# Kernel tuning notes

Hardware: AMD Instinct MI355X
Metric: run time of the kernel (lower is better)

## Reference

```python
import jax, jax.numpy as jnp
import numpy as np

N = 100000          # num nodes
E = 1600000         # num edges
EMB = 192           # embedding_dimension (divisible by 3)
THIRD = EMB // 3    # 64
NUM_REL = 2
SLOPE = 0.01        # LeakyReLU default negative slope


def leaky_relu(x):
    return jnp.where(x >= 0, x, SLOPE * x)


def setup_inputs() -> dict:
    key = jax.random.key(0)
    ks = jax.random.split(key, 20)
    s = 0.02
    inp = {
        "des": jax.random.normal(ks[0], (N, 768), jnp.float32),
        "tweet": jax.random.normal(ks[1], (N, 768), jnp.float32),
        "num_prop": jax.random.normal(ks[2], (N, 4), jnp.float32),
        "cat_prop": jax.random.normal(ks[3], (N, 3), jnp.float32),
        "edge_index": jax.random.randint(ks[4], (2, E), 0, N, jnp.int64).astype(jnp.int32),
        "edge_type": jax.random.randint(ks[5], (E,), 0, NUM_REL, jnp.int32),
        # params
        "W_des": s * jax.random.normal(ks[6], (768, THIRD), jnp.float32),
        "b_des": jnp.zeros((THIRD,), jnp.float32),
        "W_num": s * jax.random.normal(ks[7], (4, THIRD), jnp.float32),
        "b_num": jnp.zeros((THIRD,), jnp.float32),
        "W_cat": s * jax.random.normal(ks[8], (3, THIRD), jnp.float32),
        "b_cat": jnp.zeros((THIRD,), jnp.float32),
        "W_in": s * jax.random.normal(ks[9], (EMB, EMB), jnp.float32),
        "b_in": jnp.zeros((EMB,), jnp.float32),
        "W_root": s * jax.random.normal(ks[10], (EMB, EMB), jnp.float32),
        "W_rel": s * jax.random.normal(ks[11], (NUM_REL, EMB, EMB), jnp.float32),
        "b_rgcn": jnp.zeros((EMB,), jnp.float32),
        "W_o1": s * jax.random.normal(ks[12], (EMB, EMB), jnp.float32),
        "b_o1": jnp.zeros((EMB,), jnp.float32),
        "W_o2": s * jax.random.normal(ks[13], (EMB, 2), jnp.float32),
        "b_o2": jnp.zeros((2,), jnp.float32),
    }
    return inp


def rgcn_conv(x, edge_index, edge_type, W_root, W_rel, b_rgcn):
    # PyG RGCNConv (default): out = x @ W_root + b + sum_r mean_{edges r -> i}(x[src] @ W_r)
    # mean of (x_j @ W_r) == (mean of x_j) @ W_r, so aggregate first (cheaper).
    src, dst = edge_index[0], edge_index[1]
    h = x[src]  # [E, EMB] gather
    out = x @ W_root + b_rgcn
    for r in range(NUM_REL):
        m = (edge_type == r).astype(x.dtype)  # [E]
        s = jax.ops.segment_sum(h * m[:, None], dst, num_segments=N)  # [N, EMB]
        cnt = jax.ops.segment_sum(m, dst, num_segments=N)             # [N]
        agg = s / jnp.maximum(cnt, 1.0)[:, None]
        out = out + agg @ W_rel[r]
    return out


def reference(des, tweet, num_prop, cat_prop, edge_index, edge_type,
              W_des, b_des, W_num, b_num, W_cat, b_cat, W_in, b_in,
              W_root, W_rel, b_rgcn, W_o1, b_o1, W_o2, b_o2):
    d = leaky_relu(des @ W_des + b_des)
    n = leaky_relu(num_prop @ W_num + b_num)
    c = leaky_relu(cat_prop @ W_cat + b_cat)
    x = jnp.concatenate((d, n, c), axis=1)          # [N, EMB]
    x = leaky_relu(x @ W_in + b_in)
    x = rgcn_conv(x, edge_index, edge_type, W_root, W_rel, b_rgcn)
    # dropout in eval mode = identity
    x = rgcn_conv(x, edge_index, edge_type, W_root, W_rel, b_rgcn)
    x = leaky_relu(x @ W_o1 + b_o1)
    x = x @ W_o2 + b_o2                              # [N, 2]
    return x
```

## Files before the change

### kernel.cpp

```cpp
#include <hip/hip_runtime.h>

typedef _Float16 f16;
typedef _Float16 f16x4 __attribute__((ext_vector_type(4)));
typedef _Float16 f16x8 __attribute__((ext_vector_type(8)));
typedef float f32x4 __attribute__((ext_vector_type(4)));

#define LRELU(v) ((v) >= 0.f ? (v) : 0.01f * (v))

__device__ __forceinline__ int swz(int a) { return a ^ (((a >> 7) & 7) << 4); }

#define BCAP 64

__global__ __launch_bounds__(256) void setup_kernel(
    const float* __restrict__ num_prop, const float* __restrict__ cat_prop,
    const float* __restrict__ W_num, const float* __restrict__ b_num,
    const float* __restrict__ W_cat, const float* __restrict__ b_cat,
    const float* __restrict__ W_des, const float* __restrict__ W_in,
    const float* __restrict__ W_root, const float* __restrict__ W_rel,
    const float* __restrict__ W_o1,
    f16* __restrict__ x0, int* __restrict__ cursor,
    f16* __restrict__ WtDes, f16* __restrict__ WtIn, f16* __restrict__ WtR,
    f16* __restrict__ WtO1,
    int N, int nbf, int nbz)
{
  int b = blockIdx.x;
  int tid = threadIdx.x;
  if (b < nbf) {
    int w = (b * 256 + tid) >> 6;
    int lane = tid & 63;
    if (w < N) {
      const float* npr = num_prop + (size_t)w * 4;
      const float* cpr = cat_prop + (size_t)w * 3;
      float vn = b_num[lane];
#pragma unroll
      for (int k = 0; k < 4; k++) vn += npr[k] * W_num[k * 64 + lane];
      float vc = b_cat[lane];
#pragma unroll
      for (int k = 0; k < 3; k++) vc += cpr[k] * W_cat[k * 64 + lane];
      vn = LRELU(vn);
      vc = LRELU(vc);
      x0[(size_t)w * 192 + 64 + lane] = (f16)vn;
      x0[(size_t)w * 192 + 128 + lane] = (f16)vc;
    }
    return;
  }
  b -= nbf;
  if (b < nbz) {
    int i = b * 256 + tid;
    if (i < N) cursor[i] = 0;
    return;
  }
  b -= nbz;
  if (b < 192) {
    int idx = b * 256 + tid;
    if (idx < 64 * 768) { int n = idx / 768, k = idx % 768; WtDes[idx] = (f16)W_des[k * 64 + n]; }
    return;
  }
  b -= 192;
  if (b < 144) {
    int idx = b * 256 + tid;
    if (idx < 192 * 192) { int n = idx / 192, k = idx % 192; WtIn[idx] = (f16)W_in[k * 192 + n]; }
    return;
  }
  b -= 144;
  if (b < 432) {
    int idx = b * 256 + tid;
    if (idx < 192 * 576) {
      int n = idx / 576, k = idx % 576;
      int seg = k / 192, kk = k % 192;
      float v = (seg == 0) ? W_root[kk * 192 + n] : W_rel[(seg - 1) * 192 * 192 + kk * 192 + n];
      WtR[idx] = (f16)v;
    }
    return;
  }
  b -= 432;
  {
    int idx = b * 256 + tid;
    if (idx < 192 * 192) { int n = idx / 192, k = idx % 192; WtO1[idx] = (f16)W_o1[k * 192 + n]; }
  }
}

__global__ __launch_bounds__(256) void count_fill(
    const int* __restrict__ ei, const int* __restrict__ et,
    int* __restrict__ cursor, int* __restrict__ bucket, int E)
{
  int e = blockIdx.x * 256 + threadIdx.x;
  if (e >= E) return;
  int src = ei[e];
  int dst = ei[E + e];
  int r = et[e];
  int pos = atomicAdd(&cursor[dst], 1);
  if (pos < BCAP) bucket[(size_t)dst * BCAP + pos] = src | (r << 31);
}

__global__ __launch_bounds__(256) void gemm_des_kernel(
    const float* __restrict__ A, const f16* __restrict__ Bt,
    const float* __restrict__ bias, f16* __restrict__ C, int M)
{
  __shared__ f16 lA[128 * 64];
  __shared__ f16 lB[64 * 64];
  const int tid = threadIdx.x, lane = tid & 63, wid = tid >> 6;
  const int wm = wid >> 1, wn = wid & 1;
  const int m0 = blockIdx.x * 128;
  f32x4 acc[4][2] = {};
  const int arow = tid >> 1, ahalf = tid & 1;
  int agr = m0 + arow;
  if (agr >= M) agr = M - 1;
  const float* asrc = A + (size_t)agr * 768 + ahalf * 32;
  for (int k0 = 0; k0 < 768; k0 += 64) {
    {
      const float4* s4 = reinterpret_cast<const float4*>(asrc + k0);
#pragma unroll
      for (int i = 0; i < 4; i++) {
        float4 u = s4[2 * i], w = s4[2 * i + 1];
        f16x8 h;
        h[0] = (f16)u.x; h[1] = (f16)u.y; h[2] = (f16)u.z; h[3] = (f16)u.w;
        h[4] = (f16)w.x; h[5] = (f16)w.y; h[6] = (f16)w.z; h[7] = (f16)w.w;
        int boff = arow * 128 + ahalf * 64 + i * 16;
        *reinterpret_cast<f16x8*>((char*)lA + swz(boff)) = h;
      }
    }
    {
#pragma unroll
      for (int i = 0; i < 2; i++) {
        int c = tid + i * 256;
        int n = c >> 3, k8 = c & 7;
        f16x8 h = *reinterpret_cast<const f16x8*>(Bt + (size_t)n * 768 + k0 + k8 * 8);
        *reinterpret_cast<f16x8*>((char*)lB + swz(n * 128 + k8 * 16)) = h;
      }
    }
    __syncthreads();
#pragma unroll
    for (int ks = 0; ks < 2; ks++) {
      f16x8 af[4], bf[2];
#pragma unroll
      for (int fm = 0; fm < 4; fm++) {
        int row = wm * 64 + fm * 16 + (lane & 15);
        af[fm] = *reinterpret_cast<const f16x8*>((const char*)lA + swz(row * 128 + ks * 64 + (lane >> 4) * 16));
      }
#pragma unroll
      for (int fn = 0; fn < 2; fn++) {
        int nn = wn * 32 + fn * 16 + (lane & 15);
        bf[fn] = *reinterpret_cast<const f16x8*>((const char*)lB + swz(nn * 128 + ks * 64 + (lane >> 4) * 16));
      }
#pragma unroll
      for (int fm = 0; fm < 4; fm++)
#pragma unroll
        for (int fn = 0; fn < 2; fn++)
          acc[fm][fn] = __builtin_amdgcn_mfma_f32_16x16x32_f16(af[fm], bf[fn], acc[fm][fn], 0, 0, 0);
    }
    __syncthreads();
  }
#pragma unroll
  for (int fm = 0; fm < 4; fm++) {
#pragma unroll
    for (int fn = 0; fn < 2; fn++) {
      int gc = wn * 32 + fn * 16 + (lane & 15);
      float b = bias[gc];
#pragma unroll
      for (int r = 0; r < 4; r++) {
        int gr = m0 + wm * 64 + fm * 16 + (lane >> 4) * 4 + r;
        if (gr < M) {
          float v = acc[fm][fn][r] + b;
          C[(size_t)gr * 192 + gc] = (f16)LRELU(v);
        }
      }
    }
  }
}

template <int NSEG, bool RELU, bool OUT2>
__global__ __launch_bounds__(512) void gemm_x_kernel(
    const f16* __restrict__ A0, const f16* __restrict__ A1, const f16* __restrict__ A2,
    const f16* __restrict__ Bt, const float* __restrict__ bias,
    f16* __restrict__ C, int M,
    const float* __restrict__ W_o2, const float* __restrict__ b_o2,
    float* __restrict__ out)
{
  __shared__ f16 lA[128 * 64];
  __shared__ f16 lB[192 * 64];
  const int tid = threadIdx.x, lane = tid & 63, wid = tid >> 6;
  const int wm = wid >> 2, wn = wid & 3;
  const int m0 = blockIdx.x * 128;
  const int Ktot = NSEG * 192;
  f32x4 acc[4][3] = {};
  const f16* segs[3] = {A0, A1, A2};
  const int arow = tid >> 2, aq = tid & 3;
  int agr = m0 + arow;
  if (agr >= M) agr = M - 1;
  int seg = 0, kin = 0;
  for (int it = 0; it < NSEG * 3; it++) {
    {
      const f16x8* s8 = reinterpret_cast<const f16x8*>(segs[seg] + (size_t)agr * 192 + kin + aq * 16);
      f16x8 h0 = s8[0], h1 = s8[1];
      int b0 = arow * 128 + aq * 32;
      *reinterpret_cast<f16x8*>((char*)lA + swz(b0)) = h0;
      *reinterpret_cast<f16x8*>((char*)lA + swz(b0 + 16)) = h1;
    }
    {
      int kb = it * 64;
#pragma unroll
      for (int i = 0; i < 3; i++) {
        int c = tid + i * 512;
        int n = c >> 3, k8 = c & 7;
        f16x8 h = *reinterpret_cast<const f16x8*>(Bt + (size_t)n * Ktot + kb + k8 * 8);
        *reinterpret_cast<f16x8*>((char*)lB + swz(n * 128 + k8 * 16)) = h;
      }
    }
    __syncthreads();
#pragma unroll
    for (int ks = 0; ks < 2; ks++) {
      f16x8 af[4], bf[3];
#pragma unroll
      for (int fm = 0; fm < 4; fm++) {
        int row = wm * 64 + fm * 16 + (lane & 15);
        af[fm] = *reinterpret_cast<const f16x8*>((const char*)lA + swz(row * 128 + ks * 64 + (lane >> 4) * 16));
      }
#pragma unroll
      for (int fn = 0; fn < 3; fn++) {
        int nn = wn * 48 + fn * 16 + (lane & 15);
        bf[fn] = *reinterpret_cast<const f16x8*>((const char*)lB + swz(nn * 128 + ks * 64 + (lane >> 4) * 16));
      }
#pragma unroll
      for (int fm = 0; fm < 4; fm++)
#pragma unroll
        for (int fn = 0; fn < 3; fn++)
          acc[fm][fn] = __builtin_amdgcn_mfma_f32_16x16x32_f16(af[fm], bf[fn], acc[fm][fn], 0, 0, 0);
    }
    __syncthreads();
    kin += 64;
    if (kin == 192) { kin = 0; if (seg < NSEG - 1) seg++; }
  }
  if (OUT2) {
    __shared__ float red[128][2];
    for (int i = tid; i < 256; i += 512) ((float*)red)[i] = 0.f;
    __syncthreads();
    float bb[3], w2v[3][2];
#pragma unroll
    for (int fn = 0; fn < 3; fn++) {
      int gc = wn * 48 + fn * 16 + (lane & 15);
      bb[fn] = bias[gc];
      w2v[fn][0] = W_o2[gc * 2 + 0];
      w2v[fn][1] = W_o2[gc * 2 + 1];
    }
#pragma unroll
    for (int fm = 0; fm < 4; fm++) {
#pragma unroll
      for (int r = 0; r < 4; r++) {
        float p0 = 0.f, p1 = 0.f;
#pragma unroll
        for (int fn = 0; fn < 3; fn++) {
          float v = acc[fm][fn][r] + bb[fn];
          v = LRELU(v);
          p0 += v * w2v[fn][0];
          p1 += v * w2v[fn][1];
        }
#pragma unroll
        for (int m = 1; m < 16; m <<= 1) { p0 += __shfl_xor(p0, m); p1 += __shfl_xor(p1, m); }
        if ((lane & 15) == 0) {
          int lr = wm * 64 + fm * 16 + (lane >> 4) * 4 + r;
          atomicAdd(&red[lr][0], p0);
          atomicAdd(&red[lr][1], p1);
        }
      }
    }
    __syncthreads();
    if (tid < 256) {
      int gr = m0 + (tid >> 1);
      if (gr < M) out[(size_t)gr * 2 + (tid & 1)] = red[tid >> 1][tid & 1] + b_o2[tid & 1];
    }
  } else {
#pragma unroll
    for (int fm = 0; fm < 4; fm++) {
#pragma unroll
      for (int fn = 0; fn < 3; fn++) {
        int gc = wn * 48 + fn * 16 + (lane & 15);
        float b = bias[gc];
#pragma unroll
        for (int r = 0; r < 4; r++) {
          int gr = m0 + wm * 64 + fm * 16 + (lane >> 4) * 4 + r;
          if (gr < M) {
            float v = acc[fm][fn][r] + b;
            if (RELU) v = LRELU(v);
            C[(size_t)gr * 192 + gc] = (f16)v;
          }
        }
      }
    }
  }
}

__global__ __launch_bounds__(256) void agg_kernel(
    const f16* __restrict__ x, const int* __restrict__ bucket,
    const int* __restrict__ cursor,
    f16* __restrict__ agg0, f16* __restrict__ agg1, int N)
{
  int w = (blockIdx.x << 2) + (threadIdx.x >> 6);
  if (w >= N) return;
  const int lane = threadIdx.x & 63;
  const int g = lane >> 4, sub = lane & 15;
  int deg = cursor[w];
  if (deg > BCAP) deg = BCAP;
  const int4* bk4 = reinterpret_cast<const int4*>(bucket + (size_t)w * BCAP);
  float a0[12] = {}, a1[12] = {};
  float c1 = 0.f;
  int nj = (deg + 15) >> 4;
  for (int j = 0; j < nj; ++j) {
    int4 ee = bk4[j * 4 + g];
#pragma unroll
    for (int i = 0; i < 4; ++i) {
      int idx = j * 16 + g * 4 + i;
      if (idx < deg) {
        int e = (i == 0) ? ee.x : (i == 1) ? ee.y : (i == 2) ? ee.z : ee.w;
        int src = e & 0x7fffffff;
        const f16* rowp = x + (size_t)src * 192 + sub * 4;
        f16x4 v0 = *reinterpret_cast<const f16x4*>(rowp);
        f16x4 v1 = *reinterpret_cast<const f16x4*>(rowp + 64);
        f16x4 v2 = *reinterpret_cast<const f16x4*>(rowp + 128);
        float f[12];
#pragma unroll
        for (int c = 0; c < 4; ++c) {
          f[c] = (float)v0[c]; f[4 + c] = (float)v1[c]; f[8 + c] = (float)v2[c];
        }
        if (e < 0) {
          c1 += 1.f;
#pragma unroll
          for (int c = 0; c < 12; ++c) a1[c] += f[c];
        } else {
#pragma unroll
          for (int c = 0; c < 12; ++c) a0[c] += f[c];
        }
      }
    }
  }
#pragma unroll
  for (int c = 0; c < 12; ++c) {
    a0[c] += __shfl_xor(a0[c], 16); a0[c] += __shfl_xor(a0[c], 32);
    a1[c] += __shfl_xor(a1[c], 16); a1[c] += __shfl_xor(a1[c], 32);
  }
  c1 += __shfl_xor(c1, 16); c1 += __shfl_xor(c1, 32);
  float c0 = (float)deg - c1;
  float i0 = 1.f / fmaxf(c0, 1.f);
  float i1 = 1.f / fmaxf(c1, 1.f);
  if (g == 0) {
    f16x4 o0[3], o1[3];
#pragma unroll
    for (int c = 0; c < 12; ++c) {
      o0[c >> 2][c & 3] = (f16)(a0[c] * i0);
      o1[c >> 2][c & 3] = (f16)(a1[c] * i1);
    }
#pragma unroll
    for (int c = 0; c < 3; ++c) {
      *reinterpret_cast<f16x4*>(agg0 + (size_t)w * 192 + c * 64 + sub * 4) = o0[c];
      *reinterpret_cast<f16x4*>(agg1 + (size_t)w * 192 + c * 64 + sub * 4) = o1[c];
    }
  }
}

extern "C" void kernel_launch(void* const* d_in, const int* in_sizes, int n_in,
                              void* d_out, int out_size, void* d_ws, size_t ws_size,
                              hipStream_t stream)
{
  const float* des      = (const float*)d_in[0];
  const float* num_prop = (const float*)d_in[2];
  const float* cat_prop = (const float*)d_in[3];
  const int* edge_index = (const int*)d_in[4];
  const int* edge_type  = (const int*)d_in[5];
  const float* W_des = (const float*)d_in[6];
  const float* b_des = (const float*)d_in[7];
  const float* W_num = (const float*)d_in[8];
  const float* b_num = (const float*)d_in[9];
  const float* W_cat = (const float*)d_in[10];
  const float* b_cat = (const float*)d_in[11];
  const float* W_in  = (const float*)d_in[12];
  const float* b_in  = (const float*)d_in[13];
  const float* W_root= (const float*)d_in[14];
  const float* W_rel = (const float*)d_in[15];
  const float* b_rgcn= (const float*)d_in[16];
  const float* W_o1  = (const float*)d_in[17];
  const float* b_o1  = (const float*)d_in[18];
  const float* W_o2  = (const float*)d_in[19];
  const float* b_o2  = (const float*)d_in[20];
  float* out = (float*)d_out;

  const int N = in_sizes[2] / 4;
  const int E = in_sizes[5];
  (void)n_in; (void)out_size; (void)ws_size;

  char* base = (char*)d_ws;
  size_t off = 0;
  auto take = [&](size_t bytes) -> void* {
    void* p = base + off;
    off += (bytes + 255) & ~(size_t)255;
    return p;
  };
  f16* xA     = (f16*)take((size_t)N * 192 * 2);
  f16* xB     = (f16*)take((size_t)N * 192 * 2);
  f16* agg0   = (f16*)take((size_t)N * 192 * 2);
  f16* agg1   = (f16*)take((size_t)N * 192 * 2);
  int* bucket = (int*)take((size_t)N * BCAP * 4);
  int* cursor = (int*)take((size_t)N * 4);
  f16* WtDes  = (f16*)take(64 * 768 * 2);
  f16* WtIn   = (f16*)take(192 * 192 * 2);
  f16* WtR    = (f16*)take(192 * 576 * 2);
  f16* WtO1   = (f16*)take(192 * 192 * 2);

  const int nbf = (N + 3) / 4;
  const int nbz = (N + 255) / 256;
  const int nsetup = nbf + nbz + 192 + 144 + 432 + 144;
  setup_kernel<<<nsetup, 256, 0, stream>>>(
      num_prop, cat_prop, W_num, b_num, W_cat, b_cat,
      W_des, W_in, W_root, W_rel, W_o1,
      xA, cursor, WtDes, WtIn, WtR, WtO1, N, nbf, nbz);
  count_fill<<<(E + 255) / 256, 256, 0, stream>>>(edge_index, edge_type, cursor, bucket, E);
  gemm_des_kernel<<<(N + 127) / 128, 256, 0, stream>>>(des, WtDes, b_des, xA, N);
  gemm_x_kernel<1, true, false><<<(N + 127) / 128, 512, 0, stream>>>(
      xA, xA, xA, WtIn, b_in, xB, N, nullptr, nullptr, nullptr);
  agg_kernel<<<(N + 3) / 4, 256, 0, stream>>>(xB, bucket, cursor, agg0, agg1, N);
  gemm_x_kernel<3, false, false><<<(N + 127) / 128, 512, 0, stream>>>(
      xB, agg0, agg1, WtR, b_rgcn, xA, N, nullptr, nullptr, nullptr);
  agg_kernel<<<(N + 3) / 4, 256, 0, stream>>>(xA, bucket, cursor, agg0, agg1, N);
  gemm_x_kernel<3, false, false><<<(N + 127) / 128, 512, 0, stream>>>(
      xA, agg0, agg1, WtR, b_rgcn, xB, N, nullptr, nullptr, nullptr);
  gemm_x_kernel<1, false, true><<<(N + 127) / 128, 512, 0, stream>>>(
      xB, xB, xB, WtO1, b_o1, nullptr, N, W_o2, b_o2, out);
}
```

Measured before the change: 557.9 us.

## Fuse RGCN neighbor aggregation into the root/relation GEMM via shared memory

Replaces the separate aggregation kernel and the 3-segment GEMM with one kernel per RGCN layer. Each block first does the root GEMM, then gathers neighbor means one 64-column slice at a time into shared memory and runs the matching relation-weight MFMA steps. The weight layout is permuted to interleave the two relations per slice. This removes the agg0/agg1 round-trip through global memory, but it runs the gather with 8 waves per 128-row tile and stalls on syncthreads, which may lower latency hiding and occupancy for the irregular gathers.

Measured after the change: 1.499 ms. 2.69x slower.

```diff
diff --git a/kernel.cpp b/kernel.cpp
--- a/kernel.cpp
+++ b/kernel.cpp
@@ -67,8 +67,16 @@
     int idx = b * 256 + tid;
     if (idx < 192 * 576) {
       int n = idx / 576, k = idx % 576;
-      int seg = k / 192, kk = k % 192;
-      float v = (seg == 0) ? W_root[kk * 192 + n] : W_rel[(seg - 1) * 192 * 192 + kk * 192 + n];
+      float v;
+      if (k < 192) {
+        v = W_root[k * 192 + n];
+      } else {
+        int q = k - 192;
+        int p = q >> 7, r = q & 127;
+        int rel = (r >= 64) ? 1 : 0;
+        int kk = p * 64 + (r & 63);
+        v = W_rel[rel * 192 * 192 + kk * 192 + n];
+      }
       WtR[idx] = (f16)v;
     }
     return;
@@ -275,7 +283,7 @@
 #pragma unroll
       for (int fn = 0; fn < 3; fn++) {
         int gc = wn * 48 + fn * 16 + (lane & 15);
-        float b = bias[gc];
+        float b = bias[fn * 0 + gc];
 #pragma unroll
         for (int r = 0; r < 4; r++) {
           int gr = m0 + wm * 64 + fm * 16 + (lane >> 4) * 4 + r;
@@ -290,69 +298,142 @@
   }
 }
 
-__global__ __launch_bounds__(256) void agg_kernel(
-    const f16* __restrict__ x, const int* __restrict__ bucket,
-    const int* __restrict__ cursor,
-    f16* __restrict__ agg0, f16* __restrict__ agg1, int N)
+__global__ __launch_bounds__(512) void rgcn_fused_kernel(
+    const f16* __restrict__ X, const int* __restrict__ bucket,
+    const int* __restrict__ cursor, const f16* __restrict__ Bt,
+    const float* __restrict__ bias, f16* __restrict__ C, int M)
 {
-  int w = (blockIdx.x << 2) + (threadIdx.x >> 6);
-  if (w >= N) return;
-  const int lane = threadIdx.x & 63;
+  __shared__ char smem[32768 + 24576];
+  f16* lA = (f16*)smem;
+  f16* lB = (f16*)(smem + 32768);
+  const int tid = threadIdx.x, lane = tid & 63, wid = tid >> 6;
+  const int wm = wid >> 2, wn = wid & 3;
+  const int m0 = blockIdx.x * 128;
+  f32x4 acc[4][3] = {};
+  const int arow = tid >> 2, aq = tid & 3;
+  int agr = m0 + arow;
+  if (agr >= M) agr = M - 1;
   const int g = lane >> 4, sub = lane & 15;
-  int deg = cursor[w];
-  if (deg > BCAP) deg = BCAP;
-  const int4* bk4 = reinterpret_cast<const int4*>(bucket + (size_t)w * BCAP);
-  float a0[12] = {}, a1[12] = {};
-  float c1 = 0.f;
-  int nj = (deg + 15) >> 4;
-  for (int j = 0; j < nj; ++j) {
-    int4 ee = bk4[j * 4 + g];
-#pragma unroll
-    for (int i = 0; i < 4; ++i) {
-      int idx = j * 16 + g * 4 + i;
-      if (idx < deg) {
-        int e = (i == 0) ? ee.x : (i == 1) ? ee.y : (i == 2) ? ee.z : ee.w;
-        int src = e & 0x7fffffff;
-        const f16* rowp = x + (size_t)src * 192 + sub * 4;
-        f16x4 v0 = *reinterpret_cast<const f16x4*>(rowp);
-        f16x4 v1 = *reinterpret_cast<const f16x4*>(rowp + 64);
-        f16x4 v2 = *reinterpret_cast<const f16x4*>(rowp + 128);
-        float f[12];
+
+  auto stage_lB = [&](int it) {
+#pragma unroll
+    for (int i = 0; i < 3; i++) {
+      int c = tid + i * 512;
+      int n = c >> 3, k8 = c & 7;
+      f16x8 h = *reinterpret_cast<const f16x8*>(Bt + (size_t)n * 576 + it * 64 + k8 * 8);
+      *reinterpret_cast<f16x8*>((char*)lB + swz(n * 128 + k8 * 16)) = h;
+    }
+  };
+  auto mfma_step = [&](const char* abase) {
+#pragma unroll
+    for (int ks = 0; ks < 2; ks++) {
+      f16x8 af[4], bf[3];
+#pragma unroll
+      for (int fm = 0; fm < 4; fm++) {
+        int row = wm * 64 + fm * 16 + (lane & 15);
+        af[fm] = *reinterpret_cast<const f16x8*>(abase + swz(row * 128 + ks * 64 + (lane >> 4) * 16));
+      }
+#pragma unroll
+      for (int fn = 0; fn < 3; fn++) {
+        int nn = wn * 48 + fn * 16 + (lane & 15);
+        bf[fn] = *reinterpret_cast<const f16x8*>((const char*)lB + swz(nn * 128 + ks * 64 + (lane >> 4) * 16));
+      }
+#pragma unroll
+      for (int fm = 0; fm < 4; fm++)
+#pragma unroll
+        for (int fn = 0; fn < 3; fn++)
+          acc[fm][fn] = __builtin_amdgcn_mfma_f32_16x16x32_f16(af[fm], bf[fn], acc[fm][fn], 0, 0, 0);
+    }
+  };
+
+  for (int it = 0; it < 3; ++it) {
+    {
+      const f16x8* s8 = reinterpret_cast<const f16x8*>(X + (size_t)agr * 192 + it * 64 + aq * 16);
+      f16x8 h0 = s8[0], h1 = s8[1];
+      int b0 = arow * 128 + aq * 32;
+      *reinterpret_cast<f16x8*>((char*)lA + swz(b0)) = h0;
+      *reinterpret_cast<f16x8*>((char*)lA + swz(b0 + 16)) = h1;
+    }
+    stage_lB(it);
+    __syncthreads();
+    mfma_step((const char*)lA);
+    __syncthreads();
+  }
+
+  for (int p = 0; p < 3; ++p) {
+    for (int pass = 0; pass < 16; ++pass) {
+      int dl = (pass << 3) + wid;
+      int d = m0 + dl;
+      int deg = 0;
+      if (d < M) { deg = cursor[d]; if (deg > BCAP) deg = BCAP; }
+      const int4* bk4 = reinterpret_cast<const int4*>(bucket + (size_t)d * BCAP);
+      float a0[4] = {}, a1[4] = {};
+      float c1f = 0.f;
+      int nj = (deg + 15) >> 4;
+      for (int j = 0; j < nj; ++j) {
+        int4 ee = bk4[j * 4 + g];
+#pragma unroll
+        for (int i = 0; i < 4; ++i) {
+          int idx = j * 16 + g * 4 + i;
+          if (idx < deg) {
+            int e = (i == 0) ? ee.x : (i == 1) ? ee.y : (i == 2) ? ee.z : ee.w;
+            int src = e & 0x7fffffff;
+            f16x4 v = *reinterpret_cast<const f16x4*>(X + (size_t)src * 192 + p * 64 + sub * 4);
+            if (e < 0) {
+              c1f += 1.f;
+#pragma unroll
+              for (int c = 0; c < 4; ++c) a1[c] += (float)v[c];
+            } else {
+#pragma unroll
+              for (int c = 0; c < 4; ++c) a0[c] += (float)v[c];
+            }
+          }
+        }
+      }
+#pragma unroll
+      for (int c = 0; c < 4; ++c) {
+        a0[c] += __shfl_xor(a0[c], 16); a0[c] += __shfl_xor(a0[c], 32);
+        a1[c] += __shfl_xor(a1[c], 16); a1[c] += __shfl_xor(a1[c], 32);
+      }
+      c1f += __shfl_xor(c1f, 16); c1f += __shfl_xor(c1f, 32);
+      if (g == 0) {
+        float c0f = (float)deg - c1f;
+        float i0 = 1.f / fmaxf(c0f, 1.f);
+        float i1 = 1.f / fmaxf(c1f, 1.f);
+        f16x4 o0, o1;
 #pragma unroll
         for (int c = 0; c < 4; ++c) {
-          f[c] = (float)v0[c]; f[4 + c] = (float)v1[c]; f[8 + c] = (float)v2[c];
-        }
-        if (e < 0) {
-          c1 += 1.f;
-#pragma unroll
-          for (int c = 0; c < 12; ++c) a1[c] += f[c];
-        } else {
-#pragma unroll
-          for (int c = 0; c < 12; ++c) a0[c] += f[c];
-        }
-      }
-    }
-  }
-#pragma unroll
-  for (int c = 0; c < 12; ++c) {
-    a0[c] += __shfl_xor(a0[c], 16); a0[c] += __shfl_xor(a0[c], 32);
-    a1[c] += __shfl_xor(a1[c], 16); a1[c] += __shfl_xor(a1[c], 32);
-  }
-  c1 += __shfl_xor(c1, 16); c1 += __shfl_xor(c1, 32);
-  float c0 = (float)deg - c1;
-  float i0 = 1.f / fmaxf(c0, 1.f);
-  float i1 = 1.f / fmaxf(c1, 1.f);
-  if (g == 0) {
-    f16x4 o0[3], o1[3];
-#pragma unroll
-    for (int c = 0; c < 12; ++c) {
-      o0[c >> 2][c & 3] = (f16)(a0[c] * i0);
-      o1[c >> 2][c & 3] = (f16)(a1[c] * i1);
-    }
-#pragma unroll
-    for (int c = 0; c < 3; ++c) {
-      *reinterpret_cast<f16x4*>(agg0 + (size_t)w * 192 + c * 64 + sub * 4) = o0[c];
-      *reinterpret_cast<f16x4*>(agg1 + (size_t)w * 192 + c * 64 + sub * 4) = o1[c];
+          o0[c] = (f16)(a0[c] * i0);
+          o1[c] = (f16)(a1[c] * i1);
+        }
+        int boff = dl * 128 + sub * 8;
+        *reinterpret_cast<f16x4*>((char*)lA + swz(boff)) = o0;
+        *reinterpret_cast<f16x4*>((char*)lA + 16384 + swz(boff)) = o1;
+      }
+    }
+#pragma unroll
+    for (int s = 0; s < 2; ++s) {
+      stage_lB(3 + p * 2 + s);
+      __syncthreads();
+      mfma_step((const char*)lA + s * 16384);
+      __syncthreads();
+    }
+  }
+
+#pragma unroll
+  for (int fm = 0; fm < 4; fm++) {
+#pragma unroll
+    for (int fn = 0; fn < 3; fn++) {
+      int gc = wn * 48 + fn * 16 + (lane & 15);
+      float b = bias[gc];
+#pragma unroll
+      for (int r = 0; r < 4; r++) {
+        int gr = m0 + wm * 64 + fm * 16 + (lane >> 4) * 4 + r;
+        if (gr < M) {
+          float v = acc[fm][fn][r] + b;
+          C[(size_t)gr * 192 + gc] = (f16)v;
+        }
+      }
     }
   }
 }
@@ -396,8 +477,6 @@
   };
   f16* xA     = (f16*)take((size_t)N * 192 * 2);
   f16* xB     = (f16*)take((size_t)N * 192 * 2);
-  f16* agg0   = (f16*)take((size_t)N * 192 * 2);
-  f16* agg1   = (f16*)take((size_t)N * 192 * 2);
   int* bucket = (int*)take((size_t)N * BCAP * 4);
   int* cursor = (int*)take((size_t)N * 4);
   f16* WtDes  = (f16*)take(64 * 768 * 2);
@@ -416,12 +495,10 @@
   gemm_des_kernel<<<(N + 127) / 128, 256, 0, stream>>>(des, WtDes, b_des, xA, N);
   gemm_x_kernel<1, true, false><<<(N + 127) / 128, 512, 0, stream>>>(
       xA, xA, xA, WtIn, b_in, xB, N, nullptr, nullptr, nullptr);
-  agg_kernel<<<(N + 3) / 4, 256, 0, stream>>>(xB, bucket, cursor, agg0, agg1, N);
-  gemm_x_kernel<3, false, false><<<(N + 127) / 128, 512, 0, stream>>>(
-      xB, agg0, agg1, WtR, b_rgcn, xA, N, nullptr, nullptr, nullptr);
-  agg_kernel<<<(N + 3) / 4, 256, 0, stream>>>(xA, bucket, cursor, agg0, agg1, N);
-  gemm_x_kernel<3, false, false><<<(N + 127) / 128, 512, 0, stream>>>(
-      xA, agg0, agg1, WtR, b_rgcn, xB, N, nullptr, nullptr, nullptr);
+  rgcn_fused_kernel<<<(N + 127) / 128, 512, 0, stream>>>(
+      xB, bucket, cursor, WtR, b_rgcn, xA, N);
+  rgcn_fused_kernel<<<(N + 127) / 128, 512, 0, stream>>>(
+      xA, bucket, cursor, WtR, b_rgcn, xB, N);
   gemm_x_kernel<1, false, true><<<(N + 127) / 128, 512, 0, stream>>>(
       xB, xB, xB, WtO1, b_o1, nullptr, N, W_o2, b_o2, out);
 }
```

## Fuse edge bucketing into des GEMM launch and accumulate aggregation in fp16

Applied to the files above, without the earlier changes.

The edge count/fill pass and the des projection GEMM are merged into one launch, with trailing blocks doing the atomic bucket fill. This lets the atomic-heavy scatter overlap with the bandwidth-heavy GEMM and removes one launch. The aggregation kernel now accumulates neighbor rows in packed fp16 vectors instead of converting to fp32, which cuts conversion and ALU work and register use. In exchange, sums over up to 64 neighbors are less precise, and the fused kernel carries GEMM shared-memory allocation on the fill blocks, which can lower their occupancy.

Result: faster. 487.8 us (-12.6%).

```diff
diff --git a/kernel.cpp b/kernel.cpp
--- a/kernel.cpp
+++ b/kernel.cpp
@@ -8,6 +8,14 @@
 #define LRELU(v) ((v) >= 0.f ? (v) : 0.01f * (v))
 
 __device__ __forceinline__ int swz(int a) { return a ^ (((a >> 7) & 7) << 4); }
+
+__device__ __forceinline__ f16x4 shflx4(f16x4 v, int m) {
+  union { f16x4 h; int i[2]; } u;
+  u.h = v;
+  u.i[0] = __shfl_xor(u.i[0], m);
+  u.i[1] = __shfl_xor(u.i[1], m);
+  return u.h;
+}
 
 #define BCAP 64
 
@@ -80,25 +88,25 @@
   }
 }
 
-__global__ __launch_bounds__(256) void count_fill(
+__global__ __launch_bounds__(256) void cfdes_kernel(
+    const float* __restrict__ A, const f16* __restrict__ Bt,
+    const float* __restrict__ bias, f16* __restrict__ C, int M,
     const int* __restrict__ ei, const int* __restrict__ et,
-    int* __restrict__ cursor, int* __restrict__ bucket, int E)
-{
-  int e = blockIdx.x * 256 + threadIdx.x;
-  if (e >= E) return;
-  int src = ei[e];
-  int dst = ei[E + e];
-  int r = et[e];
-  int pos = atomicAdd(&cursor[dst], 1);
-  if (pos < BCAP) bucket[(size_t)dst * BCAP + pos] = src | (r << 31);
-}
-
-__global__ __launch_bounds__(256) void gemm_des_kernel(
-    const float* __restrict__ A, const f16* __restrict__ Bt,
-    const float* __restrict__ bias, f16* __restrict__ C, int M)
+    int* __restrict__ cursor, int* __restrict__ bucket, int E, int nbDES)
 {
   __shared__ f16 lA[128 * 64];
   __shared__ f16 lB[64 * 64];
+  if ((int)blockIdx.x >= nbDES) {
+    int e = ((int)blockIdx.x - nbDES) * 256 + threadIdx.x;
+    if (e < E) {
+      int src = ei[e];
+      int dst = ei[E + e];
+      int r = et[e];
+      int pos = atomicAdd(&cursor[dst], 1);
+      if (pos < BCAP) bucket[(size_t)dst * BCAP + pos] = src | (r << 31);
+    }
+    return;
+  }
   const int tid = threadIdx.x, lane = tid & 63, wid = tid >> 6;
   const int wm = wid >> 1, wn = wid & 1;
   const int m0 = blockIdx.x * 128;
@@ -302,8 +310,8 @@
   int deg = cursor[w];
   if (deg > BCAP) deg = BCAP;
   const int4* bk4 = reinterpret_cast<const int4*>(bucket + (size_t)w * BCAP);
-  float a0[12] = {}, a1[12] = {};
-  float c1 = 0.f;
+  f16x4 a0[3] = {}, a1[3] = {};
+  float c1f = 0.f;
   int nj = (deg + 15) >> 4;
   for (int j = 0; j < nj; ++j) {
     int4 ee = bk4[j * 4 + g];
@@ -317,42 +325,35 @@
         f16x4 v0 = *reinterpret_cast<const f16x4*>(rowp);
         f16x4 v1 = *reinterpret_cast<const f16x4*>(rowp + 64);
         f16x4 v2 = *reinterpret_cast<const f16x4*>(rowp + 128);
-        float f[12];
-#pragma unroll
-        for (int c = 0; c < 4; ++c) {
-          f[c] = (float)v0[c]; f[4 + c] = (float)v1[c]; f[8 + c] = (float)v2[c];
+        if (e < 0) {
+          c1f += 1.f;
+          a1[0] += v0; a1[1] += v1; a1[2] += v2;
+        } else {
+          a0[0] += v0; a0[1] += v1; a0[2] += v2;
         }
-        if (e < 0) {
-          c1 += 1.f;
-#pragma unroll
-          for (int c = 0; c < 12; ++c) a1[c] += f[c];
-        } else {
-#pragma unroll
-          for (int c = 0; c < 12; ++c) a0[c] += f[c];
-        }
-      }
-    }
-  }
-#pragma unroll
-  for (int c = 0; c < 12; ++c) {
-    a0[c] += __shfl_xor(a0[c], 16); a0[c] += __shfl_xor(a0[c], 32);
-    a1[c] += __shfl_xor(a1[c], 16); a1[c] += __shfl_xor(a1[c], 32);
-  }
-  c1 += __shfl_xor(c1, 16); c1 += __shfl_xor(c1, 32);
-  float c0 = (float)deg - c1;
-  float i0 = 1.f / fmaxf(c0, 1.f);
-  float i1 = 1.f / fmaxf(c1, 1.f);
+      }
+    }
+  }
+#pragma unroll
+  for (int c = 0; c < 3; ++c) {
+    a0[c] += shflx4(a0[c], 16); a0[c] += shflx4(a0[c], 32);
+    a1[c] += shflx4(a1[c], 16); a1[c] += shflx4(a1[c], 32);
+  }
+  c1f += __shfl_xor(c1f, 16); c1f += __shfl_xor(c1f, 32);
   if (g == 0) {
-    f16x4 o0[3], o1[3];
-#pragma unroll
-    for (int c = 0; c < 12; ++c) {
-      o0[c >> 2][c & 3] = (f16)(a0[c] * i0);
-      o1[c >> 2][c & 3] = (f16)(a1[c] * i1);
-    }
+    float c0f = (float)deg - c1f;
+    float i0 = 1.f / fmaxf(c0f, 1.f);
+    float i1 = 1.f / fmaxf(c1f, 1.f);
 #pragma unroll
     for (int c = 0; c < 3; ++c) {
-      *reinterpret_cast<f16x4*>(agg0 + (size_t)w * 192 + c * 64 + sub * 4) = o0[c];
-      *reinterpret_cast<f16x4*>(agg1 + (size_t)w * 192 + c * 64 + sub * 4) = o1[c];
+      f16x4 o0, o1;
+#pragma unroll
+      for (int k = 0; k < 4; ++k) {
+        o0[k] = (f16)((float)a0[c][k] * i0);
+        o1[k] = (f16)((float)a1[c][k] * i1);
+      }
+      *reinterpret_cast<f16x4*>(agg0 + (size_t)w * 192 + c * 64 + sub * 4) = o0;
+      *reinterpret_cast<f16x4*>(agg1 + (size_t)w * 192 + c * 64 + sub * 4) = o1;
     }
   }
 }
@@ -412,8 +413,10 @@
       num_prop, cat_prop, W_num, b_num, W_cat, b_cat,
       W_des, W_in, W_root, W_rel, W_o1,
       xA, cursor, WtDes, WtIn, WtR, WtO1, N, nbf, nbz);
-  count_fill<<<(E + 255) / 256, 256, 0, stream>>>(edge_index, edge_type, cursor, bucket, E);
-  gemm_des_kernel<<<(N + 127) / 128, 256, 0, stream>>>(des, WtDes, b_des, xA, N);
+  const int nbDES = (N + 127) / 128;
+  const int nbCF = (E + 255) / 256;
+  cfdes_kernel<<<nbDES + nbCF, 256, 0, stream>>>(
+      des, WtDes, b_des, xA, N, edge_index, edge_type, cursor, bucket, E, nbDES);
   gemm_x_kernel<1, true, false><<<(N + 127) / 128, 512, 0, stream>>>(
       xA, xA, xA, WtIn, b_in, xB, N, nullptr, nullptr, nullptr);
   agg_kernel<<<(N + 3) / 4, 256, 0, stream>>>(xB, bucket, cursor, agg0, agg1, N);
```
